# Optimization experiments

Hardware: AMD Instinct MI355X
Metric: run time of the kernel (lower is better)

Reference implementation:

```python
import jax, jax.numpy as jnp
import numpy as np

OFFSET = 1  # self.offset

def setup_inputs() -> dict:
    key = jax.random.key(0)
    k1, k2, k3, k4, k5 = jax.random.split(key, 5)
    B, D, T, S, N = 16, 512, 1024, 12, 10
    x = jax.random.normal(k1, (B, D, T), dtype=jnp.float32)
    y = jax.random.normal(k2, (B, D, T), dtype=jnp.float32)
    W = jax.random.normal(k3, (D, D, S), dtype=jnp.float32) * 0.05  # ConvTranspose2d weight [in, out, 1, steps] squeezed
    b = jax.random.normal(k4, (D,), dtype=jnp.float32) * 0.05
    neg_idxs = jax.random.randint(k5, (B, N * T), 0, T)
    return {"x": x, "y": y, "W": W, "b": b, "neg_idxs": neg_idxs}


def reference(x, y, W, b, neg_idxs):
    B, F, T = y.shape
    N = neg_idxs.shape[1] // T
    # --- sample_negatives: gather by computed index over flattened y ---
    y_flat = jnp.transpose(y, (1, 0, 2)).reshape(F, B * T)          # [F, B*T]
    idx = (neg_idxs + jnp.arange(B, dtype=neg_idxs.dtype)[:, None] * T).reshape(-1)
    negs = y_flat[:, idx].reshape(F, B, N, T).transpose(2, 1, 0, 3)  # [N, B, F, T]
    targets = jnp.concatenate([y[None], negs], axis=0)               # [C=N+1, B, F, T]
    # --- project_to_steps: ConvTranspose2d with kernel (1, steps) == per-step linear ---
    xp = jnp.einsum('bit,ios->bots', x, W) + b[None, :, None, None]  # [B, F, T, S]
    C = N + 1
    S = xp.shape[-1]
    steps = min(S, T - OFFSET)
    preds, labels = [], []
    for i in range(steps):  # small fixed loop over prediction steps
        off = i + OFFSET
        # [C, B, T-off]: dot over feature dim, copies broadcast over x
        p = jnp.einsum('bft,cbft->cbt', xp[:, :, :T - off, i], targets[:, :, :, off:])
        preds.append(p.reshape(-1))
        lab = jnp.zeros((C, B * (T - off)), dtype=xp.dtype).at[0].set(1.0)
        labels.append(lab.reshape(-1))
    predictions = jnp.concatenate(preds)
    labels_out = jnp.concatenate(labels)
    return predictions, labels_out
```

## Files before the change

### kernel.cpp

```cpp
#include <hip/hip_runtime.h>

typedef __bf16 bf16x8 __attribute__((ext_vector_type(8)));
typedef float f32x4 __attribute__((ext_vector_type(4)));

#define B_ 16
#define T_ 1024
#define D_ 512
#define S_ 12
#define C_ 11
static constexpr int P_TOTAL = 2148960;

__device__ __host__ inline constexpr int pred_base(int i) {
  return C_ * B_ * (T_ * i - (i * (i + 1)) / 2);
}

__device__ inline unsigned short f2bf(float f) {
  unsigned int u = __float_as_uint(f);
  u += 0x7FFF + ((u >> 16) & 1);
  return (unsigned short)(u >> 16);
}

__device__ inline void gld16(const void* g, void* l) {
  __builtin_amdgcn_global_load_lds(
      (const __attribute__((address_space(1))) void*)g,
      (__attribute__((address_space(3))) void*)l, 16, 0, 0);
}

__global__ __launch_bounds__(256) void prep_w(const float* __restrict__ W,
                                              unsigned short* __restrict__ wt) {
  __shared__ unsigned short tile[32][33][12];
  const int i0 = blockIdx.x * 32, o0 = blockIdx.y * 32;
#pragma unroll
  for (int q = 0; q < 48; ++q) {
    int idx = threadIdx.x + q * 256;
    int ii = idx / 384, rem = idx % 384;
    tile[ii][rem / 12][rem % 12] =
        f2bf(W[(size_t)(i0 + ii) * 6144 + (size_t)o0 * 12 + rem]);
  }
  __syncthreads();
#pragma unroll
  for (int q = 0; q < 48; ++q) {
    int idx = threadIdx.x + q * 256;
    int ss = idx / 1024, rem = idx % 1024;
    int oo = rem / 32, ii = rem % 32;
    wt[(size_t)ss * (D_ * D_) + (size_t)(o0 + oo) * D_ + (i0 + ii)] = tile[ii][oo][ss];
  }
}

__global__ __launch_bounds__(256) void prep_t2(const float* __restrict__ xin,
                                               const float* __restrict__ yin,
                                               unsigned short* __restrict__ xo,
                                               unsigned short* __restrict__ yo) {
  __shared__ float tile[32][33];
  const int t0 = blockIdx.x * 32;
  const int d0 = blockIdx.y * 32;
  const int b = blockIdx.z & 15;
  const float* in = (blockIdx.z < 16) ? xin : yin;
  unsigned short* ob = (blockIdx.z < 16) ? xo : yo;
  const float* ib = in + (size_t)b * D_ * T_;
  const int r = threadIdx.x / 32, c = threadIdx.x % 32;
#pragma unroll
  for (int p = 0; p < 4; ++p) {
    int rr = r + p * 8;
    tile[rr][c] = ib[(size_t)(d0 + rr) * T_ + t0 + c];
  }
  __syncthreads();
  unsigned short* op = ob + (size_t)b * T_ * D_;
#pragma unroll
  for (int p = 0; p < 4; ++p) {
    int rr = r + p * 8;
    op[(size_t)(t0 + rr) * D_ + d0 + c] = f2bf(tile[c][rr]);
  }
}

__global__ void labels_k(float* __restrict__ lab) {
  int k = blockIdx.x * 256 + threadIdx.x;
  if (k >= P_TOTAL) return;
  int i = 0;
#pragma unroll
  for (int q = 1; q < 12; ++q)
    if (k >= pred_base(q)) i = q;
  int rel = k - pred_base(i);
  int len = T_ - 1 - i;
  lab[k] = (rel < B_ * len) ? 1.0f : 0.0f;
}

__global__ __launch_bounds__(512, 2) void gemm_xp(
    const unsigned short* __restrict__ xb,
    const unsigned short* __restrict__ wt,
    const float* __restrict__ bias,
    unsigned short* __restrict__ xp,
    int m0_global, int tiles, int mtiles) {
  __shared__ unsigned short lds[65536];
  const int tid = threadIdx.x;
  const int w = tid >> 6, l = tid & 63;
  const int gm = w >> 2, gn = w & 3;
  const int fr = l & 15, sgrp = l >> 4;

  const int so0 = tid * 16;
  const int row0 = so0 >> 6, sc0 = (so0 >> 4) & 3;
  const int go0 = row0 * 1024 + ((sc0 ^ ((row0 >> 1) & 3)) << 4);
  const int so1 = so0 + 8192;
  const int row1 = so1 >> 6, sc1 = (so1 >> 4) & 3;
  const int go1 = row1 * 1024 + ((sc1 ^ ((row1 >> 1) & 3)) << 4);

  auto stage = [&](const unsigned short* srcKt, int slotShorts) {
    gld16((const char*)srcKt + go0, (char*)&lds[slotShorts] + so0);
    gld16((const char*)srcKt + go1, (char*)&lds[slotShorts] + so1);
  };

  auto rdfrag = [&](const unsigned short* base, int row) -> bf16x8 {
    int idx = row * 32 + ((sgrp ^ ((row >> 1) & 3)) << 3);
    return *(const bf16x8*)&base[idx];
  };

  auto decode = [&](int t, const unsigned short*& Ag, const unsigned short*& Bg,
                    int& n0v, int& miv, int& siv) {
    miv = t % mtiles;
    int rest = t / mtiles;
    int ni = rest & 1;
    siv = rest >> 1;
    Ag = xb + (size_t)(miv * 256) * D_;
    Bg = wt + ((size_t)siv * D_ + ni * 256) * D_;
    n0v = ni * 256;
  };
  (void)m0_global;

  int ti = blockIdx.x;
  if (ti >= tiles) return;
  const unsigned short *Ag, *Bg, *Agn = nullptr, *Bgn = nullptr;
  int n0, mi, si, n0n, min_, sin_;
  decode(ti, Ag, Bg, n0, mi, si);
  int tin = ti + gridDim.x;
  bool hasNext = tin < tiles;
  if (hasNext) decode(tin, Agn, Bgn, n0n, min_, sin_);

  stage(Ag, 0);
  stage(Bg, 8192);
  stage(Ag + 32, 16384);
  stage(Bg + 32, 16384 + 8192);
  asm volatile("s_waitcnt vmcnt(4)" ::: "memory");
  __builtin_amdgcn_s_barrier();

  while (true) {
    f32x4 acc[2][4][4];
#pragma unroll
    for (int ms = 0; ms < 2; ++ms)
#pragma unroll
      for (int fm = 0; fm < 4; ++fm)
#pragma unroll
        for (int fn = 0; fn < 4; ++fn)
#pragma unroll
          for (int e = 0; e < 4; ++e) acc[ms][fm][fn][e] = 0.f;

    float bv[4];
#pragma unroll
    for (int fn = 0; fn < 4; ++fn) bv[fn] = bias[n0 + gn * 64 + fn * 16 + fr];

    for (int kt = 0; kt < 16; ++kt) {
      const int sl = kt & 3;
      const unsigned short* A_l = &lds[sl * 16384];
      const unsigned short* B_l = A_l + 8192;
      const int k2 = kt + 2;
      const int sl2s = (k2 & 3) * 16384;
      const unsigned short* sA = nullptr;
      const unsigned short* sB = nullptr;
      if (k2 < 16) {
        sA = Ag + k2 * 32;
        sB = Bg + k2 * 32;
      } else if (hasNext) {
        sA = Agn + (k2 - 16) * 32;
        sB = Bgn + (k2 - 16) * 32;
      }
      bf16x8 af[4], bfr[4];

#pragma unroll
      for (int fn = 0; fn < 4; ++fn)
        bfr[fn] = rdfrag(B_l, gn * 64 + fn * 16 + fr);
#pragma unroll
      for (int fm = 0; fm < 4; ++fm)
        af[fm] = rdfrag(A_l, gm * 128 + fm * 16 + fr);
      if (sA) stage(sA, sl2s);
      __builtin_amdgcn_s_barrier();
      __builtin_amdgcn_s_setprio(1);
#pragma unroll
      for (int fm = 0; fm < 4; ++fm)
#pragma unroll
        for (int fn = 0; fn < 4; ++fn)
          acc[0][fm][fn] = __builtin_amdgcn_mfma_f32_16x16x32_bf16(
              af[fm], bfr[fn], acc[0][fm][fn], 0, 0, 0);
      __builtin_amdgcn_s_setprio(0);

#pragma unroll
      for (int fm = 0; fm < 4; ++fm)
        af[fm] = rdfrag(A_l, gm * 128 + 64 + fm * 16 + fr);
      if (sB) stage(sB, sl2s + 8192);
      asm volatile("s_waitcnt vmcnt(4)" ::: "memory");
      __builtin_amdgcn_s_barrier();
      __builtin_amdgcn_s_setprio(1);
#pragma unroll
      for (int fm = 0; fm < 4; ++fm)
#pragma unroll
        for (int fn = 0; fn < 4; ++fn)
          acc[1][fm][fn] = __builtin_amdgcn_mfma_f32_16x16x32_bf16(
              af[fm], bfr[fn], acc[1][fm][fn], 0, 0, 0);
      __builtin_amdgcn_s_setprio(0);
    }

#pragma unroll
    for (int ms = 0; ms < 2; ++ms) {
#pragma unroll
      for (int fm = 0; fm < 4; ++fm) {
#pragma unroll
        for (int r = 0; r < 4; ++r) {
          int m = mi * 256 + gm * 128 + ms * 64 + fm * 16 + sgrp * 4 + r;
          int bl = m >> 10, t = m & 1023;
          size_t orow = (((size_t)bl * S_ + si) * T_ + t) * D_;
#pragma unroll
          for (int fn = 0; fn < 4; ++fn) {
            int o = n0 + gn * 64 + fn * 16 + fr;
            xp[orow + o] = f2bf(acc[ms][fm][fn][r] + bv[fn]);
          }
        }
      }
    }

    if (!hasNext) break;
    ti = tin;
    Ag = Agn; Bg = Bgn; n0 = n0n; mi = min_; si = sin_;
    tin = ti + gridDim.x;
    hasNext = tin < tiles;
    if (hasNext) decode(tin, Agn, Bgn, n0n, min_, sin_);
  }
}

__global__ __launch_bounds__(256) void pred_k(
    const unsigned short* __restrict__ xp,
    const unsigned short* __restrict__ yT,
    const int* __restrict__ negs,
    float* __restrict__ preds, int b0) {
  const int w = threadIdx.x >> 6, l = threadIdx.x & 63;
  const int bl = blockIdx.y;
  const int b = b0 + bl;
  const int fr = l & 15;
  const int koff = (l >> 4) * 8;
  const int tta = blockIdx.x * 4 + w;
  const int ttb = tta + 512;

  int ta = tta - 1 - fr;
  bool ava = (fr < S_) && (ta >= 0);
  const unsigned short* arowA =
      xp + (((size_t)bl * S_ + (ava ? fr : 0)) * T_ + (ava ? ta : 0)) * D_;
  int tb = ttb - 1 - fr;
  bool avb = (fr < S_) && (tb >= 0);
  const unsigned short* arowB =
      xp + (((size_t)bl * S_ + (avb ? fr : 0)) * T_ + (avb ? tb : 0)) * D_;

  int ja = tta, jb = ttb;
  if (fr >= 1 && fr <= 10) {
    ja = negs[b * (10 * T_) + (fr - 1) * T_ + tta];
    jb = negs[b * (10 * T_) + (fr - 1) * T_ + ttb];
  }
  const unsigned short* browA = yT + ((size_t)b * T_ + ja) * D_;
  const unsigned short* browB = yT + ((size_t)b * T_ + jb) * D_;

  f32x4 accA, accB;
#pragma unroll
  for (int e = 0; e < 4; ++e) { accA[e] = 0.f; accB[e] = 0.f; }
#pragma unroll
  for (int kk = 0; kk < 16; ++kk) {
    bf16x8 a0 = *(const bf16x8*)(arowA + kk * 32 + koff);
    bf16x8 b0v = *(const bf16x8*)(browA + kk * 32 + koff);
    bf16x8 a1 = *(const bf16x8*)(arowB + kk * 32 + koff);
    bf16x8 b1v = *(const bf16x8*)(browB + kk * 32 + koff);
    accA = __builtin_amdgcn_mfma_f32_16x16x32_bf16(a0, b0v, accA, 0, 0, 0);
    accB = __builtin_amdgcn_mfma_f32_16x16x32_bf16(a1, b1v, accB, 0, 0, 0);
  }
#pragma unroll
  for (int r = 0; r < 4; ++r) {
    int ii = (l >> 4) * 4 + r;
    if (ii < S_ && fr < C_) {
      int len = T_ - 1 - ii;
      int toa = tta - 1 - ii;
      if (tta >= 1 && toa >= 0)
        preds[pred_base(ii) + ((size_t)fr * B_ + b) * len + toa] = accA[r];
      int tob = ttb - 1 - ii;
      if (tob >= 0)
        preds[pred_base(ii) + ((size_t)fr * B_ + b) * len + tob] = accB[r];
    }
  }
}

extern "C" void kernel_launch(void* const* d_in, const int* in_sizes, int n_in,
                              void* d_out, int out_size, void* d_ws, size_t ws_size,
                              hipStream_t stream) {
  (void)in_sizes; (void)n_in; (void)out_size;
  const float* x = (const float*)d_in[0];
  const float* y = (const float*)d_in[1];
  const float* W = (const float*)d_in[2];
  const float* bias = (const float*)d_in[3];
  const int* negs = (const int*)d_in[4];
  float* out = (float*)d_out;
  char* ws = (char*)d_ws;

  unsigned short* wt = (unsigned short*)ws;
  unsigned short* xb = (unsigned short*)(ws + 6291456);
  unsigned short* yT = (unsigned short*)(ws + 6291456 + 16777216);
  unsigned short* xp = (unsigned short*)(ws + 6291456 + 2 * 16777216);
  const size_t fixed = 6291456 + (size_t)2 * 16777216;
  const size_t xp_per_b = (size_t)S_ * T_ * D_ * 2;
  int nb = 1;
  if (ws_size > fixed) {
    size_t cap = (ws_size - fixed) / xp_per_b;
    nb = cap < 1 ? 1 : (cap > 16 ? 16 : (int)cap);
  }

  hipLaunchKernelGGL(prep_w, dim3(16, 16), dim3(256), 0, stream, W, wt);
  hipLaunchKernelGGL(prep_t2, dim3(32, 16, 32), dim3(256), 0, stream, x, y, xb, yT);
  hipLaunchKernelGGL(labels_k, dim3((P_TOTAL + 255) / 256), dim3(256), 0, stream,
                     out + P_TOTAL);

  for (int b0 = 0; b0 < B_; b0 += nb) {
    int bc = (B_ - b0) < nb ? (B_ - b0) : nb;
    int tiles = bc * 4 * 2 * 12;
    int grid = tiles < 256 ? tiles : 256;
    hipLaunchKernelGGL(gemm_xp, dim3(grid), dim3(512), 0, stream,
                       xb + (size_t)b0 * T_ * D_, wt, bias, xp, b0 * T_,
                       tiles, bc * 4);
    hipLaunchKernelGGL(pred_k, dim3(128, bc), dim3(256), 0, stream,
                       xp, yT, negs, out, b0);
  }
}
```

Measured before the change: 216.3 us.

## Software-pipeline LDS fragment reads in GEMM and widen pred kernel per-wave work

The GEMM main loop now double-buffers register fragments: fragments for the next k-step are read from LDS after the barrier and overlap the second MFMA half, both global-to-LDS stages are issued together, one barrier is dropped per iteration, and LDS offsets are precomputed. The pred kernel handles four time positions per wave instead of two, halving its grid so more loads are in flight per wave. The aim is to hide LDS latency and cut synchronisation in the GEMM and raise memory-level parallelism in the gather-dot kernel. The trade-off is higher register pressure, which could lower occupancy, and more complex wait-count logic at tile boundaries.

```diff
diff --git a/kernel.cpp b/kernel.cpp
--- a/kernel.cpp
+++ b/kernel.cpp
@@ -90,7 +90,7 @@
     const unsigned short* __restrict__ wt,
     const float* __restrict__ bias,
     unsigned short* __restrict__ xp,
-    int m0_global, int tiles, int mtiles) {
+    int tiles, int mtiles) {
   __shared__ unsigned short lds[65536];
   const int tid = threadIdx.x;
   const int w = tid >> 6, l = tid & 63;
@@ -109,10 +109,19 @@
     gld16((const char*)srcKt + go1, (char*)&lds[slotShorts] + so1);
   };
 
-  auto rdfrag = [&](const unsigned short* base, int row) -> bf16x8 {
-    int idx = row * 32 + ((sgrp ^ ((row >> 1) & 3)) << 3);
-    return *(const bf16x8*)&base[idx];
-  };
+  int aOff[2][4], bOff[4];
+#pragma unroll
+  for (int ms = 0; ms < 2; ++ms)
+#pragma unroll
+    for (int fm = 0; fm < 4; ++fm) {
+      int row = gm * 128 + ms * 64 + fm * 16 + fr;
+      aOff[ms][fm] = row * 32 + ((sgrp ^ ((row >> 1) & 3)) << 3);
+    }
+#pragma unroll
+  for (int fn = 0; fn < 4; ++fn) {
+    int row = gn * 64 + fn * 16 + fr;
+    bOff[fn] = row * 32 + ((sgrp ^ ((row >> 1) & 3)) << 3);
+  }
 
   auto decode = [&](int t, const unsigned short*& Ag, const unsigned short*& Bg,
                     int& n0v, int& miv, int& siv) {
@@ -124,7 +133,6 @@
     Bg = wt + ((size_t)siv * D_ + ni * 256) * D_;
     n0v = ni * 256;
   };
-  (void)m0_global;
 
   int ti = blockIdx.x;
   if (ti >= tiles) return;
@@ -142,6 +150,14 @@
   asm volatile("s_waitcnt vmcnt(4)" ::: "memory");
   __builtin_amdgcn_s_barrier();
 
+  bf16x8 afA[4], bfrA[4];
+#pragma unroll
+  for (int fn = 0; fn < 4; ++fn)
+    bfrA[fn] = *(const bf16x8*)&lds[8192 + bOff[fn]];
+#pragma unroll
+  for (int fm = 0; fm < 4; ++fm)
+    afA[fm] = *(const bf16x8*)&lds[aOff[0][fm]];
+
   while (true) {
     f32x4 acc[2][4][4];
 #pragma unroll
@@ -157,54 +173,70 @@
 #pragma unroll
     for (int fn = 0; fn < 4; ++fn) bv[fn] = bias[n0 + gn * 64 + fn * 16 + fr];
 
+#pragma unroll
     for (int kt = 0; kt < 16; ++kt) {
-      const int sl = kt & 3;
-      const unsigned short* A_l = &lds[sl * 16384];
-      const unsigned short* B_l = A_l + 8192;
+      const int sl = (kt & 3) * 16384;
+      bf16x8 afB[4];
+#pragma unroll
+      for (int fm = 0; fm < 4; ++fm)
+        afB[fm] = *(const bf16x8*)&lds[sl + aOff[1][fm]];
+
       const int k2 = kt + 2;
-      const int sl2s = (k2 & 3) * 16384;
-      const unsigned short* sA = nullptr;
-      const unsigned short* sB = nullptr;
+      const int sl2 = (k2 & 3) * 16384;
+      bool st = false;
       if (k2 < 16) {
-        sA = Ag + k2 * 32;
-        sB = Bg + k2 * 32;
+        stage(Ag + k2 * 32, sl2);
+        stage(Bg + k2 * 32, sl2 + 8192);
+        st = true;
       } else if (hasNext) {
-        sA = Agn + (k2 - 16) * 32;
-        sB = Bgn + (k2 - 16) * 32;
-      }
-      bf16x8 af[4], bfr[4];
-
-#pragma unroll
-      for (int fn = 0; fn < 4; ++fn)
-        bfr[fn] = rdfrag(B_l, gn * 64 + fn * 16 + fr);
-#pragma unroll
-      for (int fm = 0; fm < 4; ++fm)
-        af[fm] = rdfrag(A_l, gm * 128 + fm * 16 + fr);
-      if (sA) stage(sA, sl2s);
-      __builtin_amdgcn_s_barrier();
+        stage(Agn + (k2 - 16) * 32, sl2);
+        stage(Bgn + (k2 - 16) * 32, sl2 + 8192);
+        st = true;
+      }
+
       __builtin_amdgcn_s_setprio(1);
 #pragma unroll
       for (int fm = 0; fm < 4; ++fm)
 #pragma unroll
         for (int fn = 0; fn < 4; ++fn)
           acc[0][fm][fn] = __builtin_amdgcn_mfma_f32_16x16x32_bf16(
-              af[fm], bfr[fn], acc[0][fm][fn], 0, 0, 0);
+              afA[fm], bfrA[fn], acc[0][fm][fn], 0, 0, 0);
       __builtin_amdgcn_s_setprio(0);
 
-#pragma unroll
-      for (int fm = 0; fm < 4; ++fm)
-        af[fm] = rdfrag(A_l, gm * 128 + 64 + fm * 16 + fr);
-      if (sB) stage(sB, sl2s + 8192);
-      asm volatile("s_waitcnt vmcnt(4)" ::: "memory");
+      if (st) {
+        asm volatile("s_waitcnt vmcnt(4)" ::: "memory");
+      } else if (kt == 14) {
+        asm volatile("s_waitcnt vmcnt(0)" ::: "memory");
+      }
       __builtin_amdgcn_s_barrier();
+
+      bf16x8 afN[4], bfN[4];
+      const bool pre = (kt < 15) || hasNext;
+      if (pre) {
+        const int nsl = ((kt + 1) & 3) * 16384;
+#pragma unroll
+        for (int fn = 0; fn < 4; ++fn)
+          bfN[fn] = *(const bf16x8*)&lds[nsl + 8192 + bOff[fn]];
+#pragma unroll
+        for (int fm = 0; fm < 4; ++fm)
+          afN[fm] = *(const bf16x8*)&lds[nsl + aOff[0][fm]];
+      }
+
       __builtin_amdgcn_s_setprio(1);
 #pragma unroll
       for (int fm = 0; fm < 4; ++fm)
 #pragma unroll
         for (int fn = 0; fn < 4; ++fn)
           acc[1][fm][fn] = __builtin_amdgcn_mfma_f32_16x16x32_bf16(
-              af[fm], bfr[fn], acc[1][fm][fn], 0, 0, 0);
+              afB[fm], bfrA[fn], acc[1][fm][fn], 0, 0, 0);
       __builtin_amdgcn_s_setprio(0);
+
+      if (pre) {
+#pragma unroll
+        for (int fm = 0; fm < 4; ++fm) afA[fm] = afN[fm];
+#pragma unroll
+        for (int fn = 0; fn < 4; ++fn) bfrA[fn] = bfN[fn];
+      }
     }
 
 #pragma unroll
@@ -244,49 +276,48 @@
   const int b = b0 + bl;
   const int fr = l & 15;
   const int koff = (l >> 4) * 8;
-  const int tta = blockIdx.x * 4 + w;
-  const int ttb = tta + 512;
-
-  int ta = tta - 1 - fr;
-  bool ava = (fr < S_) && (ta >= 0);
-  const unsigned short* arowA =
-      xp + (((size_t)bl * S_ + (ava ? fr : 0)) * T_ + (ava ? ta : 0)) * D_;
-  int tb = ttb - 1 - fr;
-  bool avb = (fr < S_) && (tb >= 0);
-  const unsigned short* arowB =
-      xp + (((size_t)bl * S_ + (avb ? fr : 0)) * T_ + (avb ? tb : 0)) * D_;
-
-  int ja = tta, jb = ttb;
-  if (fr >= 1 && fr <= 10) {
-    ja = negs[b * (10 * T_) + (fr - 1) * T_ + tta];
-    jb = negs[b * (10 * T_) + (fr - 1) * T_ + ttb];
-  }
-  const unsigned short* browA = yT + ((size_t)b * T_ + ja) * D_;
-  const unsigned short* browB = yT + ((size_t)b * T_ + jb) * D_;
-
-  f32x4 accA, accB;
-#pragma unroll
-  for (int e = 0; e < 4; ++e) { accA[e] = 0.f; accB[e] = 0.f; }
+
+  const unsigned short* arow[4];
+  const unsigned short* brow[4];
+  int tts[4];
+#pragma unroll
+  for (int q = 0; q < 4; ++q) {
+    int tt = blockIdx.x * 4 + w + q * 256;
+    tts[q] = tt;
+    int t = tt - 1 - fr;
+    bool av = (fr < S_) && (t >= 0);
+    arow[q] = xp + (((size_t)bl * S_ + (av ? fr : 0)) * T_ + (av ? t : 0)) * D_;
+    int j = tt;
+    if (fr >= 1 && fr <= 10) j = negs[b * (10 * T_) + (fr - 1) * T_ + tt];
+    brow[q] = yT + ((size_t)b * T_ + j) * D_;
+  }
+
+  f32x4 acc[4];
+#pragma unroll
+  for (int q = 0; q < 4; ++q)
+#pragma unroll
+    for (int e = 0; e < 4; ++e) acc[q][e] = 0.f;
+
 #pragma unroll
   for (int kk = 0; kk < 16; ++kk) {
-    bf16x8 a0 = *(const bf16x8*)(arowA + kk * 32 + koff);
-    bf16x8 b0v = *(const bf16x8*)(browA + kk * 32 + koff);
-    bf16x8 a1 = *(const bf16x8*)(arowB + kk * 32 + koff);
-    bf16x8 b1v = *(const bf16x8*)(browB + kk * 32 + koff);
-    accA = __builtin_amdgcn_mfma_f32_16x16x32_bf16(a0, b0v, accA, 0, 0, 0);
-    accB = __builtin_amdgcn_mfma_f32_16x16x32_bf16(a1, b1v, accB, 0, 0, 0);
-  }
-#pragma unroll
-  for (int r = 0; r < 4; ++r) {
-    int ii = (l >> 4) * 4 + r;
-    if (ii < S_ && fr < C_) {
-      int len = T_ - 1 - ii;
-      int toa = tta - 1 - ii;
-      if (tta >= 1 && toa >= 0)
-        preds[pred_base(ii) + ((size_t)fr * B_ + b) * len + toa] = accA[r];
-      int tob = ttb - 1 - ii;
-      if (tob >= 0)
-        preds[pred_base(ii) + ((size_t)fr * B_ + b) * len + tob] = accB[r];
+#pragma unroll
+    for (int q = 0; q < 4; ++q) {
+      bf16x8 a = *(const bf16x8*)(arow[q] + kk * 32 + koff);
+      bf16x8 bb = *(const bf16x8*)(brow[q] + kk * 32 + koff);
+      acc[q] = __builtin_amdgcn_mfma_f32_16x16x32_bf16(a, bb, acc[q], 0, 0, 0);
+    }
+  }
+
+#pragma unroll
+  for (int q = 0; q < 4; ++q) {
+#pragma unroll
+    for (int r = 0; r < 4; ++r) {
+      int ii = (l >> 4) * 4 + r;
+      int to = tts[q] - 1 - ii;
+      if (ii < S_ && fr < C_ && tts[q] >= 1 && to >= 0) {
+        int len = T_ - 1 - ii;
+        preds[pred_base(ii) + ((size_t)fr * B_ + b) * len + to] = acc[q][r];
+      }
     }
   }
 }
@@ -325,9 +356,9 @@
     int tiles = bc * 4 * 2 * 12;
     int grid = tiles < 256 ? tiles : 256;
     hipLaunchKernelGGL(gemm_xp, dim3(grid), dim3(512), 0, stream,
-                       xb + (size_t)b0 * T_ * D_, wt, bias, xp, b0 * T_,
+                       xb + (size_t)b0 * T_ * D_, wt, bias, xp,
                        tiles, bc * 4);
-    hipLaunchKernelGGL(pred_k, dim3(128, bc), dim3(256), 0, stream,
+    hipLaunchKernelGGL(pred_k, dim3(64, bc), dim3(256), 0, stream,
                        xp, yT, negs, out, b0);
   }
 }
```

Measured after the change: 220.6 us. About the same (+2.0%).
